# Optimization experiments

Hardware: AMD Instinct MI355X
Metric: run time of the kernel (lower is better)

## Reference

```python
import jax, jax.numpy as jnp
import numpy as np

V, N, K, D = 2, 100000, 8, 128
TAU = 1.0
LOG_2PI = float(np.log(2.0 * np.pi))


def setup_inputs() -> dict:
    key = jax.random.key(0)
    k1, k2, k3 = jax.random.split(key, 3)
    z = jax.random.normal(k1, (V, N, D), dtype=jnp.float32)
    phi = jnp.ones((V, K), dtype=jnp.float32) / K
    mu = jax.random.normal(k2, (V, K, D), dtype=jnp.float32)
    # sigma: identity (as in torch init) plus a small symmetric PSD perturbation
    a = 0.05 * jax.random.normal(k3, (V, K, D, D), dtype=jnp.float32)
    sigma = jnp.eye(D, dtype=jnp.float32) + jnp.einsum('vkde,vkfe->vkdf', a, a)
    return {"z": z, "phi": phi, "mu": mu, "sigma": sigma}


def _compute_energy(z, phi, mu, sigma):
    # z: [N, D]; phi: [K]; mu: [K, D]; sigma: [K, D, D]
    eps_eye = 1e-6 * jnp.eye(D, dtype=z.dtype)
    sigma_stable = sigma + eps_eye  # [K, D, D]
    inv_sigma = jnp.linalg.inv(sigma_stable)
    det_sigma = jnp.clip(jnp.linalg.det(sigma_stable), 1e-6, None)  # [K]
    diff = z[:, None, :] - mu[None, :, :]  # [N, K, D]
    maha = jnp.einsum('nkd,kde,nke->nk', diff, inv_sigma, diff)  # [N, K]
    log_pi = jax.nn.log_softmax(phi)  # [K]
    log_prob = (-0.5 * maha
                - 0.5 * D * LOG_2PI
                - 0.5 * jnp.log(det_sigma)[None, :]
                + log_pi[None, :])  # [N, K]
    energy = -jax.nn.logsumexp(log_prob, axis=1)  # [N]
    penalty = jnp.sum(1.0 / (jnp.diagonal(sigma_stable, axis1=-2, axis2=-1) + 1e-12))
    return energy, penalty


def reference(z, phi, mu, sigma):
    # vmap over views; energies_v: [V, N]
    energies_v, penalties = jax.vmap(_compute_energy)(z, phi, mu, sigma)
    energies = energies_v.T  # [N, V]
    total_energies = jnp.sum(energies)
    total_penalty = jnp.sum(penalties)
    weights = jax.nn.softmax(-energies / TAU, axis=1)  # [N, V]
    return energies, weights, total_energies, total_penalty
```

## Files before the change

### kernel.cpp

```cpp
#include <hip/hip_runtime.h>
#include <math.h>

#define V 2
#define NN 100000
#define KK 8
#define DD 128
#define TILE_N 128
#define SL 132
#define NT 782
#define CH 7
#define CPX 14
#define NPAD 100096
#define LOG2PI 1.8378770664093454f
#define LOG_1EM6 -13.815510557964274f

#define IMG_PB 40960
#define IMG_LO_US 10240

#define LF_B   1114112
#define LF_STRIDE 69632
#define BV_B   2228224
#define C_B    2236416
#define MAHA_B 2236480

#define OUT_W_OFF (NN*V)
#define OUT_TE (2*NN*V)
#define OUT_TP (2*NN*V + 1)

typedef __attribute__((ext_vector_type(8)))  short bf16x8;
typedef __attribute__((ext_vector_type(4)))  float f32x4;
typedef __attribute__((ext_vector_type(16))) float f32x16;
typedef __attribute__((ext_vector_type(4)))  unsigned u32x4;

__device__ __forceinline__ unsigned short f2bf_rtn(float f) {
    unsigned u = __builtin_bit_cast(unsigned, f);
    unsigned r = u + 0x7FFFu + ((u >> 16) & 1u);
    return (unsigned short)(r >> 16);
}
__device__ __forceinline__ float bf2f(unsigned short h) {
    unsigned u = ((unsigned)h) << 16;
    return __builtin_bit_cast(float, u);
}

__device__ __forceinline__ void cvt_pair(float f0, float f1, unsigned& hi, unsigned& lo) {
    unsigned u0 = __builtin_bit_cast(unsigned, f0);
    unsigned u1 = __builtin_bit_cast(unsigned, f1);
    hi = __builtin_amdgcn_perm(u1, u0, 0x07060302u);
    float r0 = f0 - __builtin_bit_cast(float, u0 & 0xFFFF0000u);
    float r1 = f1 - __builtin_bit_cast(float, u1 & 0xFFFF0000u);
    unsigned v0 = __builtin_bit_cast(unsigned, r0) + 0x8000u;
    unsigned v1 = __builtin_bit_cast(unsigned, r1) + 0x8000u;
    lo = __builtin_amdgcn_perm(v1, v0, 0x07060302u);
}

__global__ void zero_kernel(float* out) {
    int t = threadIdx.x;
    if (t < 2) out[OUT_TE + t] = 0.0f;
}

__global__ __launch_bounds__(256) void prep_chol(const float* __restrict__ phi,
                                                 const float* __restrict__ mu,
                                                 const float* __restrict__ sigma,
                                                 void* __restrict__ wsv,
                                                 float* __restrict__ out) {
    __shared__ float Lf[DD * SL];
    __shared__ float P[8][SL];
    __shared__ float dvec[DD];
    __shared__ float mulds[DD];
    __shared__ float red[256];
    __shared__ float Bv[8];
    __shared__ float Bb[DD];

    const int tid = threadIdx.x;
    const int vk  = blockIdx.x;
    const int v   = vk >> 3;
    const int k   = vk & 7;
    const int R   = tid >> 4;
    const int C   = tid & 15;

    if (tid < DD) mulds[tid] = mu[vk * DD + tid];

    float A[8][8];
    const float* sig = sigma + (size_t)vk * DD * DD;
    float pen = 0.0f;
    #pragma unroll
    for (int a = 0; a < 8; ++a) {
        const float4* p4 = (const float4*)(sig + (size_t)(8 * R + a) * DD + 8 * C);
        float4 x = p4[0], y = p4[1];
        A[a][0] = x.x; A[a][1] = x.y; A[a][2] = x.z; A[a][3] = x.w;
        A[a][4] = y.x; A[a][5] = y.y; A[a][6] = y.z; A[a][7] = y.w;
        if (R == C) A[a][a] += 1e-6f;
    }
    if (R == C) {
        #pragma unroll
        for (int a = 0; a < 8; ++a) pen += 1.0f / (A[a][a] + 1e-12f);
    }

    for (int i = tid; i < DD * SL; i += 256) Lf[i] = 0.0f;

    red[tid] = pen;
    __syncthreads();
    for (int s = 128; s > 0; s >>= 1) {
        if (tid < s) red[tid] += red[tid + s];
        __syncthreads();
    }
    if (tid == 0) atomicAdd(&out[OUT_TP], red[0]);
    __syncthreads();

    for (int p = 0; p < 16; ++p) {
        if (C == p && R >= p) {
            #pragma unroll
            for (int b = 0; b < 8; ++b) {
                *(float4*)&P[b][8 * R]     = make_float4(A[0][b], A[1][b], A[2][b], A[3][b]);
                *(float4*)&P[b][8 * R + 4] = make_float4(A[4][b], A[5][b], A[6][b], A[7][b]);
            }
        }
        __syncthreads();

        if (tid < 64) {
            const int lane = tid;
            const int r1 = 8 * p + lane;
            const int r2 = r1 + 64;
            const bool ok2 = (r2 < DD);
            float pr1[8], pr2[8], rs[8];
            #pragma unroll
            for (int j = 0; j < 8; ++j) {
                pr1[j] = (r1 < DD) ? P[j][r1] : 0.0f;
                pr2[j] = ok2 ? P[j][r2] : 0.0f;
            }
            #pragma unroll
            for (int j = 0; j < 8; ++j) {
                if (lane >= j && lane < 8) Bv[lane] = pr1[j];
                __builtin_amdgcn_wave_barrier();
                float bv[8];
                #pragma unroll
                for (int m = 0; m < 8; ++m) bv[m] = Bv[m];
                __builtin_amdgcn_wave_barrier();
                float piv = bv[j];
                if (lane == j) dvec[8 * p + j] = piv;
                float inv2 = 1.0f / piv;
                rs[j] = rsqrtf(piv);
                float m1 = pr1[j] * inv2;
                float m2 = pr2[j] * inv2;
                #pragma unroll
                for (int j2 = 0; j2 < 8; ++j2) {
                    if (j2 > j) {
                        if (lane > j) pr1[j2] -= m1 * bv[j2];
                        pr2[j2] -= m2 * bv[j2];
                    }
                }
            }
            #pragma unroll
            for (int j = 0; j < 8; ++j) {
                if (r1 < DD) {
                    float v1 = (lane >= j) ? pr1[j] * rs[j] : 0.0f;
                    P[j][r1] = v1;
                    Lf[r1 * SL + 8 * p + j] = v1;
                }
                if (ok2) {
                    float v2 = pr2[j] * rs[j];
                    P[j][r2] = v2;
                    Lf[r2 * SL + 8 * p + j] = v2;
                }
            }
        }
        __syncthreads();

        if (C > p && R >= p) {
            #pragma unroll
            for (int j = 0; j < 8; ++j) {
                float4 a0 = *(const float4*)&P[j][8 * R];
                float4 a1 = *(const float4*)&P[j][8 * R + 4];
                float4 b0 = *(const float4*)&P[j][8 * C];
                float4 b1 = *(const float4*)&P[j][8 * C + 4];
                float ra[8] = {a0.x, a0.y, a0.z, a0.w, a1.x, a1.y, a1.z, a1.w};
                float rb[8] = {b0.x, b0.y, b0.z, b0.w, b1.x, b1.y, b1.z, b1.w};
                #pragma unroll
                for (int a = 0; a < 8; ++a)
                    #pragma unroll
                    for (int b = 0; b < 8; ++b)
                        A[a][b] -= ra[a] * rb[b];
            }
        }
        __syncthreads();
    }

    if (tid < 64) {
        const int lane = tid;
        float acc0 = mulds[lane];
        float acc1 = mulds[lane + 64];
        for (int j = 0; j < DD; ++j) {
            if (j < 64) { if (lane == j)      Bb[j] = acc0 / Lf[j * SL + j]; }
            else        { if (lane == j - 64) Bb[j] = acc1 / Lf[j * SL + j]; }
            __builtin_amdgcn_wave_barrier();
            float bj = Bb[j];
            __builtin_amdgcn_wave_barrier();
            if (lane > j)      acc0 -= Lf[lane * SL + j] * bj;
            if (lane + 64 > j) acc1 -= Lf[(lane + 64) * SL + j] * bj;
        }
    }
    __syncthreads();
    if (tid < DD) ((float*)((char*)wsv + BV_B))[vk * DD + tid] = Bb[tid];

    {
        float4* Lg = (float4*)((char*)wsv + LF_B + (size_t)vk * LF_STRIDE);
        const float4* Ls4 = (const float4*)Lf;
        for (int i = tid; i < DD * SL / 4; i += 256) Lg[i] = Ls4[i];
    }

    red[tid] = (tid < DD) ? logf(dvec[tid]) : 0.0f;
    __syncthreads();
    for (int s = 128; s > 0; s >>= 1) {
        if (tid < s) red[tid] += red[tid + s];
        __syncthreads();
    }
    if (tid == 0) {
        float logdet_c = fmaxf(red[0], LOG_1EM6);
        const float* ph = phi + v * KK;
        float m = ph[0];
        for (int i = 1; i < KK; ++i) m = fmaxf(m, ph[i]);
        float s = 0.0f;
        for (int i = 0; i < KK; ++i) s += expf(ph[i] - m);
        float logpi = ph[k] - m - logf(s);
        ((float*)((char*)wsv + C_B))[vk] = logpi - 0.5f * logdet_c - 0.5f * (float)DD * LOG2PI;
    }
}

__global__ __launch_bounds__(256) void prep_trsm(void* __restrict__ wsv) {
    __shared__ float Ls[DD * SL];
    __shared__ float Wc[32][SL];

    const int tid = threadIdx.x;
    const int vk  = blockIdx.x >> 2;
    const int cg  = blockIdx.x & 3;

    const float4* Lg = (const float4*)((const char*)wsv + LF_B + (size_t)vk * LF_STRIDE);
    float4* Ls4 = (float4*)Ls;
    for (int i = tid; i < DD * SL / 4; i += 256) Ls4[i] = Lg[i];
    __syncthreads();

    const int c   = tid >> 3;
    const int par = tid & 7;
    const int j   = 4 * c + cg;

    for (int e = par; e < SL; e += 8) Wc[c][e] = 0.0f;
    if (par == 0) Wc[c][j] = 1.0f / Ls[j * SL + j];
    __builtin_amdgcn_wave_barrier();

    const int pbase = j & ~3;
    for (int i = j + 1; i < DD; ++i) {
        float s = 0.0f;
        for (int p4 = pbase + 4 * par; p4 < i; p4 += 32) {
            float4 lf = *(const float4*)&Ls[i * SL + p4];
            float4 wc = *(const float4*)&Wc[c][p4];
            s += lf.x * wc.x + lf.y * wc.y + lf.z * wc.z + lf.w * wc.w;
        }
        s += __shfl_xor(s, 1, 64);
        s += __shfl_xor(s, 2, 64);
        s += __shfl_xor(s, 4, 64);
        if (par == 0) Wc[c][i] = -s / Ls[i * SL + i];
        __builtin_amdgcn_wave_barrier();
    }

    unsigned short* Gh = (unsigned short*)((char*)wsv + (size_t)vk * IMG_PB);
    for (int i2 = par; i2 < DD; i2 += 8) {
        const int b = i2 >> 5;
        if ((j >> 5) > b) continue;
        const int rl   = i2 & 31;
        const int hbus = (b == 0 ? 0 : b == 1 ? 1024 : b == 2 ? 3072 : 6144);
        const int us   = hbus + (j >> 3) * 256 + rl * 8 + (j & 7);
        float f = (i2 >= j) ? Wc[c][i2] : 0.0f;
        unsigned short hsh = f2bf_rtn(f);
        unsigned short lsh = f2bf_rtn(f - bf2f(hsh));
        Gh[us] = hsh;
        Gh[us + IMG_LO_US] = lsh;
    }
}

__global__ __launch_bounds__(256) void maha_kernel(const float* __restrict__ z,
                                                   void* __restrict__ wsv) {
    __shared__ unsigned short wl[IMG_PB / 2];
    __shared__ float bl_s[DD];

    const int tid  = threadIdx.x;
    const int lane = tid & 63;
    const int wave = tid >> 6;
    const int rl   = lane & 31;
    const int h    = lane >> 5;

    const int bi    = blockIdx.x;
    const int xcd   = bi & 7;
    const int jj    = bi >> 3;
    const int r     = jj & 15;
    const int lc    = jj >> 4;
    const int chunk = xcd * CPX + lc;
    const int vv    = r >> 3;

    {
        const char* src = (const char*)wsv + (size_t)r * IMG_PB;
        char* dst = (char*)wl;
        const int lane_off = wave * 1024 + lane * 16;
        #pragma unroll
        for (int t = 0; t < 10; ++t)
            __builtin_amdgcn_global_load_lds(
                (const __attribute__((address_space(1))) void*)(src + t * 4096 + lane_off),
                (__attribute__((address_space(3))) void*)(dst + t * 4096 + wave * 1024),
                16, 0, 0);
    }
    if (tid < DD) bl_s[tid] = ((const float*)((const char*)wsv + BV_B))[r * DD + tid];
    __syncthreads();

    const float* zbase = z + (size_t)vv * NN * DD;
    float* mrow = (float*)((char*)wsv + MAHA_B) + (size_t)r * NPAD;
    const char* wlb = (const char*)wl + (h * 512 + rl * 16);

    for (int ti = 0; ti < CH; ++ti) {
        const int t = chunk * CH + ti;
        if (t >= NT) break;
        const int n0 = t * TILE_N;

        const int n   = n0 + wave * 32 + rl;
        const bool ok = (n < NN);
        const float* zp = zbase + (size_t)n * DD + h * 8;

        float4 raw[8][2];
        #pragma unroll
        for (int s = 0; s < 8; ++s) {
            if (ok) {
                raw[s][0] = *(const float4*)(zp + s * 16);
                raw[s][1] = *(const float4*)(zp + s * 16 + 4);
            } else {
                raw[s][0] = make_float4(0.f, 0.f, 0.f, 0.f);
                raw[s][1] = make_float4(0.f, 0.f, 0.f, 0.f);
            }
        }

        u32x4 zh8[8], zl8[8];
        #pragma unroll
        for (int s = 0; s < 8; ++s) {
            float4 a = raw[s][0];
            float4 b = raw[s][1];
            unsigned h0, l0, h1, l1, h2, l2, h3, l3;
            cvt_pair(a.x, a.y, h0, l0);
            cvt_pair(a.z, a.w, h1, l1);
            cvt_pair(b.x, b.y, h2, l2);
            cvt_pair(b.z, b.w, h3, l3);
            u32x4 th, tl;
            th[0] = h0; th[1] = h1; th[2] = h2; th[3] = h3;
            tl[0] = l0; tl[1] = l1; tl[2] = l2; tl[3] = l3;
            zh8[s] = th;
            zl8[s] = tl;
        }

        float pa = 0.0f;
        #pragma unroll
        for (int R = 0; R < 4; ++R) {
            const int hb = (R == 0 ? 0 : R == 1 ? 2048 : R == 2 ? 6144 : 12288);
            f32x16 D = (f32x16)(0.0f);
            #pragma unroll
            for (int s = 0; s <= 2 * R + 1; ++s) {
                const int off = hb + 1024 * s;
                bf16x8 wh  = *(const bf16x8*)(wlb + off);
                bf16x8 wlo = *(const bf16x8*)(wlb + off + 2 * IMG_LO_US);
                bf16x8 zh = __builtin_bit_cast(bf16x8, zh8[s]);
                bf16x8 zl = __builtin_bit_cast(bf16x8, zl8[s]);
                D = __builtin_amdgcn_mfma_f32_32x32x16_bf16(wh,  zh, D, 0, 0, 0);
                D = __builtin_amdgcn_mfma_f32_32x32x16_bf16(wlo, zh, D, 0, 0, 0);
                D = __builtin_amdgcn_mfma_f32_32x32x16_bf16(wh,  zl, D, 0, 0, 0);
            }
            #pragma unroll
            for (int q = 0; q < 4; ++q) {
                float4 bq = *(const float4*)&bl_s[32 * R + 8 * q + 4 * h];
                float t0 = D[4 * q + 0] - bq.x;
                float t1 = D[4 * q + 1] - bq.y;
                float t2 = D[4 * q + 2] - bq.z;
                float t3 = D[4 * q + 3] - bq.w;
                pa += t0 * t0 + t1 * t1 + t2 * t2 + t3 * t3;
            }
        }

        pa += __shfl_xor(pa, 32, 64);
        if (lane < 32) mrow[n0 + wave * 32 + rl] = pa;
    }
}

__global__ __launch_bounds__(256) void finalize_kernel(const void* __restrict__ wsv,
                                                       float* __restrict__ out) {
    __shared__ float red[256];
    __shared__ float clds[16];

    const int tid = threadIdx.x;
    if (tid < 16) clds[tid] = ((const float*)((const char*)wsv + C_B))[tid];
    __syncthreads();

    const float* mahap = (const float*)((const char*)wsv + MAHA_B);
    const int n = blockIdx.x * 256 + tid;
    float esum = 0.0f;

    if (n < NN) {
        float ev[V];
        #pragma unroll
        for (int vv = 0; vv < V; ++vv) {
            float lp[KK];
            float m = -1e30f;
            #pragma unroll
            for (int k = 0; k < KK; ++k) {
                int r = vv * KK + k;
                lp[k] = -0.5f * mahap[(size_t)r * NPAD + n] + clds[r];
                m = fmaxf(m, lp[k]);
            }
            float s = 0.0f;
            #pragma unroll
            for (int k = 0; k < KK; ++k) s += expf(lp[k] - m);
            ev[vv] = -(m + logf(s));
        }
        float e0 = ev[0], e1 = ev[1];
        float m = fmaxf(-e0, -e1);
        float x0 = expf(-e0 - m);
        float x1 = expf(-e1 - m);
        float inv = 1.0f / (x0 + x1);
        out[(size_t)n * V + 0] = e0;
        out[(size_t)n * V + 1] = e1;
        out[OUT_W_OFF + (size_t)n * V + 0] = x0 * inv;
        out[OUT_W_OFF + (size_t)n * V + 1] = x1 * inv;
        esum = e0 + e1;
    }

    red[tid] = esum;
    __syncthreads();
    for (int s = 128; s > 0; s >>= 1) {
        if (tid < s) red[tid] += red[tid + s];
        __syncthreads();
    }
    if (tid == 0) atomicAdd(&out[OUT_TE], red[0]);
}

extern "C" void kernel_launch(void* const* d_in, const int* in_sizes, int n_in,
                              void* d_out, int out_size, void* d_ws, size_t ws_size,
                              hipStream_t stream) {
    const float* z     = (const float*)d_in[0];
    const float* phi   = (const float*)d_in[1];
    const float* mu    = (const float*)d_in[2];
    const float* sigma = (const float*)d_in[3];
    float* out = (float*)d_out;

    hipLaunchKernelGGL(zero_kernel, dim3(1), dim3(64), 0, stream, out);
    hipLaunchKernelGGL(prep_chol, dim3(V * KK), dim3(256), 0, stream, phi, mu, sigma, d_ws, out);
    hipLaunchKernelGGL(prep_trsm, dim3(64), dim3(256), 0, stream, d_ws);
    hipLaunchKernelGGL(maha_kernel, dim3(8 * CPX * 16), dim3(256), 0, stream, z, d_ws);
    hipLaunchKernelGGL(finalize_kernel, dim3((NPAD + 255) / 256), dim3(256), 0, stream, d_ws, out);
}
```

Baseline: 369.9 us.

## Drop zero kernel, use hardware bf16 convert, read bias from global, early-exit idle blocks

Removes the separate zero kernel. The energy total is now cleared inside prep_chol, and the penalty sum is written per block to workspace and reduced deterministically in finalize. The bf16 hi/lo split uses the v_cvt_pk_bf16_f32 instruction instead of manual perm and bit masking, which changes rounding of the high part to round-to-nearest. The per-row bias vector is loaded from global memory per tile instead of staged through LDS, and blocks with no tiles to process return early. The aim is to cut one launch and some ALU/LDS work, but zeroing OUT_TE in block 0 of prep_chol relies on ordering against the finalize atomics.

```diff
diff --git a/kernel.cpp b/kernel.cpp
--- a/kernel.cpp
+++ b/kernel.cpp
@@ -22,6 +22,7 @@
 #define BV_B   2228224
 #define C_B    2236416
 #define MAHA_B 2236480
+#define PEN_B  8642624
 
 #define OUT_W_OFF (NN*V)
 #define OUT_TE (2*NN*V)
@@ -43,19 +44,16 @@
 }
 
 __device__ __forceinline__ void cvt_pair(float f0, float f1, unsigned& hi, unsigned& lo) {
-    unsigned u0 = __builtin_bit_cast(unsigned, f0);
-    unsigned u1 = __builtin_bit_cast(unsigned, f1);
-    hi = __builtin_amdgcn_perm(u1, u0, 0x07060302u);
-    float r0 = f0 - __builtin_bit_cast(float, u0 & 0xFFFF0000u);
-    float r1 = f1 - __builtin_bit_cast(float, u1 & 0xFFFF0000u);
-    unsigned v0 = __builtin_bit_cast(unsigned, r0) + 0x8000u;
-    unsigned v1 = __builtin_bit_cast(unsigned, r1) + 0x8000u;
-    lo = __builtin_amdgcn_perm(v1, v0, 0x07060302u);
-}
-
-__global__ void zero_kernel(float* out) {
-    int t = threadIdx.x;
-    if (t < 2) out[OUT_TE + t] = 0.0f;
+    unsigned hp;
+    asm("v_cvt_pk_bf16_f32 %0, %1, %2" : "=v"(hp) : "v"(f0), "v"(f1));
+    float h0 = __builtin_bit_cast(float, hp << 16);
+    float h1 = __builtin_bit_cast(float, hp & 0xFFFF0000u);
+    float r0 = f0 - h0;
+    float r1 = f1 - h1;
+    unsigned lp;
+    asm("v_cvt_pk_bf16_f32 %0, %1, %2" : "=v"(lp) : "v"(r0), "v"(r1));
+    hi = hp;
+    lo = lp;
 }
 
 __global__ __launch_bounds__(256) void prep_chol(const float* __restrict__ phi,
@@ -78,6 +76,7 @@
     const int R   = tid >> 4;
     const int C   = tid & 15;
 
+    if (vk == 0 && tid == 0) out[OUT_TE] = 0.0f;
     if (tid < DD) mulds[tid] = mu[vk * DD + tid];
 
     float A[8][8];
@@ -104,7 +103,7 @@
         if (tid < s) red[tid] += red[tid + s];
         __syncthreads();
     }
-    if (tid == 0) atomicAdd(&out[OUT_TP], red[0]);
+    if (tid == 0) ((float*)((char*)wsv + PEN_B))[vk] = red[0];
     __syncthreads();
 
     for (int p = 0; p < 16; ++p) {
@@ -280,7 +279,6 @@
 __global__ __launch_bounds__(256) void maha_kernel(const float* __restrict__ z,
                                                    void* __restrict__ wsv) {
     __shared__ unsigned short wl[IMG_PB / 2];
-    __shared__ float bl_s[DD];
 
     const int tid  = threadIdx.x;
     const int lane = tid & 63;
@@ -296,6 +294,8 @@
     const int chunk = xcd * CPX + lc;
     const int vv    = r >> 3;
 
+    if (chunk * CH >= NT) return;
+
     {
         const char* src = (const char*)wsv + (size_t)r * IMG_PB;
         char* dst = (char*)wl;
@@ -307,10 +307,10 @@
                 (__attribute__((address_space(3))) void*)(dst + t * 4096 + wave * 1024),
                 16, 0, 0);
     }
-    if (tid < DD) bl_s[tid] = ((const float*)((const char*)wsv + BV_B))[r * DD + tid];
     __syncthreads();
 
     const float* zbase = z + (size_t)vv * NN * DD;
+    const float* bvg = (const float*)((const char*)wsv + BV_B) + r * DD + 4 * h;
     float* mrow = (float*)((char*)wsv + MAHA_B) + (size_t)r * NPAD;
     const char* wlb = (const char*)wl + (h * 512 + rl * 16);
 
@@ -356,6 +356,10 @@
         #pragma unroll
         for (int R = 0; R < 4; ++R) {
             const int hb = (R == 0 ? 0 : R == 1 ? 2048 : R == 2 ? 6144 : 12288);
+            float4 bq0 = *(const float4*)(bvg + 32 * R);
+            float4 bq1 = *(const float4*)(bvg + 32 * R + 8);
+            float4 bq2 = *(const float4*)(bvg + 32 * R + 16);
+            float4 bq3 = *(const float4*)(bvg + 32 * R + 24);
             f32x16 D = (f32x16)(0.0f);
             #pragma unroll
             for (int s = 0; s <= 2 * R + 1; ++s) {
@@ -368,13 +372,15 @@
                 D = __builtin_amdgcn_mfma_f32_32x32x16_bf16(wlo, zh, D, 0, 0, 0);
                 D = __builtin_amdgcn_mfma_f32_32x32x16_bf16(wh,  zl, D, 0, 0, 0);
             }
-            #pragma unroll
-            for (int q = 0; q < 4; ++q) {
-                float4 bq = *(const float4*)&bl_s[32 * R + 8 * q + 4 * h];
-                float t0 = D[4 * q + 0] - bq.x;
-                float t1 = D[4 * q + 1] - bq.y;
-                float t2 = D[4 * q + 2] - bq.z;
-                float t3 = D[4 * q + 3] - bq.w;
+            {
+                float t0, t1, t2, t3;
+                t0 = D[0]  - bq0.x; t1 = D[1]  - bq0.y; t2 = D[2]  - bq0.z; t3 = D[3]  - bq0.w;
+                pa += t0 * t0 + t1 * t1 + t2 * t2 + t3 * t3;
+                t0 = D[4]  - bq1.x; t1 = D[5]  - bq1.y; t2 = D[6]  - bq1.z; t3 = D[7]  - bq1.w;
+                pa += t0 * t0 + t1 * t1 + t2 * t2 + t3 * t3;
+                t0 = D[8]  - bq2.x; t1 = D[9]  - bq2.y; t2 = D[10] - bq2.z; t3 = D[11] - bq2.w;
+                pa += t0 * t0 + t1 * t1 + t2 * t2 + t3 * t3;
+                t0 = D[12] - bq3.x; t1 = D[13] - bq3.y; t2 = D[14] - bq3.z; t3 = D[15] - bq3.w;
                 pa += t0 * t0 + t1 * t1 + t2 * t2 + t3 * t3;
             }
         }
@@ -392,6 +398,14 @@
     const int tid = threadIdx.x;
     if (tid < 16) clds[tid] = ((const float*)((const char*)wsv + C_B))[tid];
     __syncthreads();
+
+    if (blockIdx.x == 0 && tid == 0) {
+        const float* pp = (const float*)((const char*)wsv + PEN_B);
+        float s = 0.0f;
+        #pragma unroll
+        for (int i = 0; i < 16; ++i) s += pp[i];
+        out[OUT_TP] = s;
+    }
 
     const float* mahap = (const float*)((const char*)wsv + MAHA_B);
     const int n = blockIdx.x * 256 + tid;
@@ -444,7 +458,6 @@
     const float* sigma = (const float*)d_in[3];
     float* out = (float*)d_out;
 
-    hipLaunchKernelGGL(zero_kernel, dim3(1), dim3(64), 0, stream, out);
     hipLaunchKernelGGL(prep_chol, dim3(V * KK), dim3(256), 0, stream, phi, mu, sigma, d_ws, out);
     hipLaunchKernelGGL(prep_trsm, dim3(64), dim3(256), 0, stream, d_ws);
     hipLaunchKernelGGL(maha_kernel, dim3(8 * CPX * 16), dim3(256), 0, stream, z, d_ws);
```

Result: slower. 386.1 us (+4.4%).
